# Performance work log

Measured on AMD Instinct MI355X. Metric: run time of the kernel, lower is better.

## Reference

```python
import jax, jax.numpy as jnp
import numpy as np

VOCAB = 32000
EMB = 10
HID = 256
CLS = 10
B = 1024
T = 256


def setup_inputs() -> dict:
    key = jax.random.key(0)
    ks = jax.random.split(key, 12)
    def w(k, shape):
        fan_in = shape[1]  # torch kaiming_normal_ (fan_in = size(1), gain=1 for 'linear')
        return jax.random.normal(k, shape, dtype=jnp.float32) / jnp.sqrt(jnp.float32(fan_in))
    inp = {
        "x": jax.random.randint(ks[0], (B, 1, T), 0, VOCAB, dtype=jnp.int32),
        "emb": jax.random.normal(ks[1], (VOCAB, EMB), dtype=jnp.float32),
        "Wgx": w(ks[2], (EMB, HID)), "Wgh": w(ks[3], (HID, HID)), "bg": jnp.zeros((HID,), jnp.float32),
        "Wix": w(ks[4], (EMB, HID)), "Wih": w(ks[5], (HID, HID)), "bi": jnp.zeros((HID,), jnp.float32),
        "Wfx": w(ks[6], (EMB, HID)), "Wfh": w(ks[7], (HID, HID)), "bf": jnp.zeros((HID,), jnp.float32),
        "Wox": w(ks[8], (EMB, HID)), "Woh": w(ks[9], (HID, HID)), "bo": jnp.zeros((HID,), jnp.float32),
        "Wph": w(ks[10], (HID, CLS)), "bp": jnp.zeros((CLS,), jnp.float32),
    }
    return inp


def reference(x, emb, Wgx, Wgh, bg, Wix, Wih, bi, Wfx, Wfh, bf, Wox, Woh, bo, Wph, bp):
    # Fuse the 4 gate projections into single matmuls (same math, concatenated).
    Wx = jnp.concatenate([Wgx, Wix, Wfx, Wox], axis=1)  # [EMB, 4H]
    Wh = jnp.concatenate([Wgh, Wih, Wfh, Woh], axis=1)  # [HID, 4H]
    b = jnp.concatenate([bg, bi, bf, bo], axis=0)       # [4H]
    H = Wgh.shape[0]
    tokens = x[:, 0, :].T  # [T, B] int

    def step(carry, tok_t):
        h, c = carry
        x_t = emb[tok_t]                       # [B, EMB]
        z = x_t @ Wx + h @ Wh + b              # [B, 4H]
        g = jnp.tanh(z[:, 0 * H:1 * H])
        i = jax.nn.sigmoid(z[:, 1 * H:2 * H])
        f = jax.nn.sigmoid(z[:, 2 * H:3 * H])
        o = jax.nn.sigmoid(z[:, 3 * H:4 * H])
        c = g * i + c * f
        h = jnp.tanh(c) * o
        return (h, c), None

    Bn = x.shape[0]
    h0 = jnp.zeros((Bn, H), dtype=emb.dtype)
    c0 = jnp.zeros((Bn, H), dtype=emb.dtype)
    (h, c), _ = jax.lax.scan(step, (h0, c0), tokens)
    return h @ Wph + bp  # [B, num_classes]
```

## Files before the change

### kernel.cpp

```cpp
#include <hip/hip_runtime.h>
#include <stdint.h>

#define T_STEPS 256
#define EMBD 10
#define NKIT 9
#define NBLK_K1 (64 * NKIT)
#define NBLK 256

typedef __attribute__((ext_vector_type(8))) short bf16x8;
typedef __attribute__((ext_vector_type(4))) float f32x4;
typedef __attribute__((ext_vector_type(4))) int   i32x4;

__device__ __forceinline__ unsigned short f2bf(float f) {
    union { float f; unsigned int u; } v; v.f = f;
    unsigned int u = v.u;
    unsigned int r = (u + 0x7FFFu + ((u >> 16) & 1u)) >> 16;
    return (unsigned short)r;
}
__device__ __forceinline__ float sig_fast(float x) {
    return __builtin_amdgcn_rcpf(1.0f + __builtin_amdgcn_exp2f(-1.4426950408889634f * x));
}
__device__ __forceinline__ float tanh_fast(float x) {
    return 1.0f - 2.0f * __builtin_amdgcn_rcpf(__builtin_amdgcn_exp2f(2.8853900817779268f * x) + 1.0f);
}
__device__ __forceinline__ f32x4 mfma_v(i32x4 a, i32x4 b, f32x4 c) {
    return __builtin_amdgcn_mfma_f32_16x16x32_bf16(
        __builtin_bit_cast(bf16x8, a), __builtin_bit_cast(bf16x8, b), c, 0, 0, 0);
}

__global__ __launch_bounds__(64) void build_wswz(
    const float* __restrict__ Wgx, const float* __restrict__ Wgh, const float* __restrict__ bg,
    const float* __restrict__ Wix, const float* __restrict__ Wih, const float* __restrict__ bi,
    const float* __restrict__ Wfx, const float* __restrict__ Wfh, const float* __restrict__ bf_,
    const float* __restrict__ Wox, const float* __restrict__ Woh, const float* __restrict__ bo,
    unsigned short* __restrict__ wswz, unsigned int* __restrict__ hxcz)
{
    {
        int4 z4 = {0, 0, 0, 0};
        size_t gid = (size_t)blockIdx.x * 64 + threadIdx.x;
        for (size_t i = gid; i < 131072; i += (size_t)NBLK_K1 * 64)
            ((int4*)hxcz)[i] = z4;
    }

    int g   = blockIdx.x / NKIT;
    int kit = blockIdx.x % NKIT;
    int lane = threadIdx.x;
    int n = g * 16 + (lane & 15);
    int q = n >> 8;
    int col = n & 255;
    const float* Wh = (q == 0) ? Wgh : (q == 1) ? Wih : (q == 2) ? Wfh : Woh;
    const float* Wx = (q == 0) ? Wgx : (q == 1) ? Wix : (q == 2) ? Wfx : Wox;
    const float* bb = (q == 0) ? bg  : (q == 1) ? bi  : (q == 2) ? bf_ : bo;
    int k0 = kit * 32 + (lane >> 4) * 8;

    int4 out;
    unsigned short* p = (unsigned short*)&out;
#pragma unroll
    for (int jx = 0; jx < 8; jx++) {
        int k = k0 + jx;
        float v = 0.0f;
        if (k < 256)             v = Wh[k * 256 + col];
        else if (k < 256 + EMBD) v = Wx[(k - 256) * 256 + col];
        else if (k == 266)       v = bb[col];
        p[jx] = f2bf(v);
    }
    ((int4*)wswz)[(kit * 64 + g) * 64 + lane] = out;
}

__global__ __launch_bounds__(512, 4)
void lstm_main(
    const int*   __restrict__ xtok,
    const float* __restrict__ emb,
    const float* __restrict__ Wph,
    const float* __restrict__ bp,
    const unsigned short* __restrict__ wswz,
    unsigned long long* __restrict__ hxc,
    float* __restrict__ out)
{
    __shared__ __align__(16) unsigned short A8_lds[2][64 * 8];
    __shared__ __align__(16) i32x4 B_lds[2 * 16 * 64];
    __shared__ __align__(16) unsigned int Ah_lds[16 * 132];
    __shared__ float z_lds[4 * 16 * 66];
    __shared__ float outacc[160];

    const int tid  = threadIdx.x;
    const int w    = tid >> 6;
    const int lane = tid & 63;
    const int blk  = blockIdx.x;
    const int gb   = blk & 63;
    const int hg   = blk >> 6;

    const int gate = w & 3;
    const int ntl0 = (w >> 2) * 2;

    const int m_x = tid >> 4;
    const int e_x = tid & 15;

    const int r_gm = tid >> 5;
    const int hc0  = (tid * 2) & 63;

    const i32x4* Bg = (const i32x4*)wswz;

    i32x4 breg[7][2];
    {
        const int ks[7] = {0, 1, 2, 3, 4, 7, 8};
#pragma unroll
        for (int i = 0; i < 7; i++)
#pragma unroll
            for (int jj = 0; jj < 2; jj++) {
                int ntile = gate * 16 + hg * 4 + ntl0 + jj;
                breg[i][jj] = Bg[(ks[i] * 64 + ntile) * 64 + lane];
            }
    }
    for (int i = tid; i < 2 * 16 * 64; i += 512) {
        int k   = i >> 10;
        int ntl = (i >> 6) & 15;
        int ln  = i & 63;
        int gt = ntl >> 2, j = ntl & 3;
        B_lds[i] = Bg[((5 + k) * 64 + gt * 16 + hg * 4 + j) * 64 + ln];
    }

    {
        int4 z4 = {0, 0, 0, 0};
        if (tid < 128) ((int4*)A8_lds)[tid] = z4;
    }
    __syncthreads();
    if (tid < 16) {
        A8_lds[0][(16 + tid) * 8 + 2] = 0x3F80;
        A8_lds[1][(16 + tid) * 8 + 2] = 0x3F80;
    }
    if (tid < 256 && e_x < EMBD) {
        int tok = xtok[(gb * 16 + m_x) * T_STEPS + 0];
        float v = emb[tok * EMBD + e_x];
        A8_lds[0][(m_x + 16 * (e_x >> 3)) * 8 + (e_x & 7)] = f2bf(v);
    }
    __syncthreads();

    float c0 = 0.0f, c1 = 0.0f;

    const int ah_rd = (lane & 15) * 33 + (lane >> 4);
    const int s_row  = tid >> 5;
    const int s_pair = tid & 31;
    const int rq0 = (hg + 1) & 3, rq1 = (hg + 2) & 3, rq2 = (hg + 3) & 3;

    for (int t = 0; t < T_STEPS; t++) {
        const int p = t & 1, q = (t + 1) & 1;

        float xval = 0.0f;
        const bool do_x = (t < T_STEPS - 1) && (tid < 256) && (e_x < EMBD);
        if ((t < T_STEPS - 1) && (tid < 256)) {
            int tok = xtok[(gb * 16 + m_x) * T_STEPS + (t + 1)];
            if (e_x < EMBD) xval = emb[tok * EMBD + e_x];
        }

        if (t > 0) {
            const unsigned long long* hb = hxc + (size_t)(p * 64 + gb) * 2048;
            const unsigned long long* a0 = hb + s_row * 128 + rq0 * 32 + s_pair;
            const unsigned long long* a1 = hb + s_row * 128 + rq1 * 32 + s_pair;
            const unsigned long long* a2 = hb + s_row * 128 + rq2 * 32 + s_pair;
            unsigned long long v0, v1, v2;
            asm volatile("global_load_dwordx2 %0, %3, off sc1\n\t"
                         "global_load_dwordx2 %1, %4, off sc1\n\t"
                         "global_load_dwordx2 %2, %5, off sc1\n\t"
                         "s_waitcnt vmcnt(0)"
                         : "=&v"(v0), "=&v"(v1), "=&v"(v2)
                         : "v"(a0), "v"(a1), "v"(a2) : "memory");
            int spins = 0;
            while ((unsigned int)(v0 >> 32) != (unsigned int)t && spins < 200000) {
                __builtin_amdgcn_s_sleep(1); ++spins;
                asm volatile("global_load_dwordx2 %0, %1, off sc1\n\ts_waitcnt vmcnt(0)"
                             : "=v"(v0) : "v"(a0) : "memory");
            }
            while ((unsigned int)(v1 >> 32) != (unsigned int)t && spins < 200000) {
                __builtin_amdgcn_s_sleep(1); ++spins;
                asm volatile("global_load_dwordx2 %0, %1, off sc1\n\ts_waitcnt vmcnt(0)"
                             : "=v"(v1) : "v"(a1) : "memory");
            }
            while ((unsigned int)(v2 >> 32) != (unsigned int)t && spins < 200000) {
                __builtin_amdgcn_s_sleep(1); ++spins;
                asm volatile("global_load_dwordx2 %0, %1, off sc1\n\ts_waitcnt vmcnt(0)"
                             : "=v"(v2) : "v"(a2) : "memory");
            }
            Ah_lds[s_row * 132 + rq0 * 32 + s_pair] = (unsigned int)v0;
            Ah_lds[s_row * 132 + rq1 * 32 + s_pair] = (unsigned int)v1;
            Ah_lds[s_row * 132 + rq2 * 32 + s_pair] = (unsigned int)v2;
        }
        __syncthreads();

        i32x4 af[8];
        if (t > 0) {
#pragma unroll
            for (int s = 0; s < 8; s++)
                af[s] = ((const i32x4*)Ah_lds)[ah_rd + s * 4];
        } else {
#pragma unroll
            for (int s = 0; s < 8; s++) af[s] = (i32x4){0, 0, 0, 0};
        }

        f32x4 acc0 = (f32x4){0.f, 0.f, 0.f, 0.f};
        f32x4 acc1 = (f32x4){0.f, 0.f, 0.f, 0.f};
        {
            i32x4 a8 = ((const i32x4*)A8_lds[p])[lane];
            acc0 = mfma_v(a8, breg[6][0], acc0);
            acc1 = mfma_v(a8, breg[6][1], acc1);
        }
        {
            const int ks6[6] = {0, 1, 2, 3, 4, 7};
#pragma unroll
            for (int i = 0; i < 6; i++) {
                acc0 = mfma_v(af[ks6[i]], breg[i][0], acc0);
                acc1 = mfma_v(af[ks6[i]], breg[i][1], acc1);
            }
        }
#pragma unroll
        for (int k = 0; k < 2; k++) {
            acc0 = mfma_v(af[5 + k], B_lds[(k * 16 + gate * 4 + ntl0 + 0) * 64 + lane], acc0);
            acc1 = mfma_v(af[5 + k], B_lds[(k * 16 + gate * 4 + ntl0 + 1) * 64 + lane], acc1);
        }

        {
            const int col = lane & 15, qd = lane >> 4;
#pragma unroll
            for (int rr = 0; rr < 4; rr++) {
                z_lds[(gate * 16 + qd * 4 + rr) * 66 + (ntl0 + 0) * 16 + col] = acc0[rr];
                z_lds[(gate * 16 + qd * 4 + rr) * 66 + (ntl0 + 1) * 16 + col] = acc1[rr];
            }
        }
        __syncthreads();

        float zg[4], zh[4];
#pragma unroll
        for (int g = 0; g < 4; g++) {
            const float2 zz = *(const float2*)&z_lds[(g * 16 + r_gm) * 66 + hc0];
            zg[g] = zz.x; zh[g] = zz.y;
        }
        float hh0, hh1;
        {
            float gg = tanh_fast(zg[0]), ii = sig_fast(zg[1]);
            float ff = sig_fast(zg[2]),  oo = sig_fast(zg[3]);
            float cn = gg * ii + c0 * ff; c0 = cn;
            hh0 = tanh_fast(cn) * oo;
        }
        {
            float gg = tanh_fast(zh[0]), ii = sig_fast(zh[1]);
            float ff = sig_fast(zh[2]),  oo = sig_fast(zh[3]);
            float cn = gg * ii + c1 * ff; c1 = cn;
            hh1 = tanh_fast(cn) * oo;
        }

        if (t < T_STEPS - 1) {
            unsigned int hp;
            asm("v_cvt_pk_bf16_f32 %0, %1, %2" : "=v"(hp) : "v"(hh0), "v"(hh1));
            Ah_lds[r_gm * 132 + hg * 32 + (hc0 >> 1)] = hp;
            if (do_x)
                A8_lds[q][(m_x + 16 * (e_x >> 3)) * 8 + (e_x & 7)] = f2bf(xval);
            unsigned long long pv =
                ((unsigned long long)(unsigned int)(t + 1) << 32) | (unsigned long long)hp;
            unsigned long long* dst =
                hxc + (size_t)(q * 64 + gb) * 2048 + r_gm * 128 + hg * 32 + (hc0 >> 1);
            asm volatile("global_store_dwordx2 %0, %1, off sc1"
                         :: "v"(dst), "v"(pv) : "memory");
        } else {
            if (tid < 160) outacc[tid] = 0.0f;
            __syncthreads();
            const int hcg = hg * 64 + hc0;
            float part[10];
#pragma unroll
            for (int cl = 0; cl < 10; cl++)
                part[cl] = hh0 * Wph[hcg * 10 + cl] + hh1 * Wph[(hcg + 1) * 10 + cl];
#pragma unroll
            for (int cl = 0; cl < 10; cl++)
                atomicAdd(&outacc[r_gm * 10 + cl], part[cl]);
            __syncthreads();
            if (tid < 160) {
                int m = tid / 10, cl = tid - m * 10;
                float v = outacc[tid];
                if (hg == 0) v += bp[cl];
                atomicAdd(&out[(gb * 16 + m) * 10 + cl], v);
            }
        }
    }
}

extern "C" void kernel_launch(void* const* d_in, const int* in_sizes, int n_in,
                              void* d_out, int out_size, void* d_ws, size_t ws_size,
                              hipStream_t stream) {
    const int*   x    = (const int*)  d_in[0];
    const float* emb  = (const float*)d_in[1];
    const float* Wgx  = (const float*)d_in[2];
    const float* Wgh  = (const float*)d_in[3];
    const float* bg   = (const float*)d_in[4];
    const float* Wix  = (const float*)d_in[5];
    const float* Wih  = (const float*)d_in[6];
    const float* bi   = (const float*)d_in[7];
    const float* Wfx  = (const float*)d_in[8];
    const float* Wfh  = (const float*)d_in[9];
    const float* bf_  = (const float*)d_in[10];
    const float* Wox  = (const float*)d_in[11];
    const float* Woh  = (const float*)d_in[12];
    const float* bo   = (const float*)d_in[13];
    const float* Wph  = (const float*)d_in[14];
    const float* bp   = (const float*)d_in[15];

    char* ws = (char*)d_ws;
    unsigned short*     wswz = (unsigned short*)ws;
    unsigned long long* hxc  = (unsigned long long*)(ws + 589824 + 4096);

    build_wswz<<<NBLK_K1, 64, 0, stream>>>(Wgx, Wgh, bg, Wix, Wih, bi,
                                           Wfx, Wfh, bf_, Wox, Woh, bo,
                                           wswz, (unsigned int*)hxc);
    lstm_main<<<NBLK, 512, 0, stream>>>(x, emb, Wph, bp, wswz, hxc,
                                        (float*)d_out);
}
```

Before: 585.3 us.

## Overlap cross-block h polling with MFMAs on locally produced hidden slice

```diff
diff --git a/kernel.cpp b/kernel.cpp
--- a/kernel.cpp
+++ b/kernel.cpp
@@ -66,6 +66,14 @@
     }
     ((int4*)wswz)[(kit * 64 + g) * 64 + lane] = out;
 }
+
+#define KIDX(s) ((s) == 7 ? 5 : (s))
+#define BSRC(s, j) ((s) == 5 ? B_lds[(0 * 16 + gate * 4 + ntl0 + (j)) * 64 + lane] \
+                  : (s) == 6 ? B_lds[(1 * 16 + gate * 4 + ntl0 + (j)) * 64 + lane] \
+                  : breg[KIDX(s)][(j)])
+#define DO_KIT(s) do { i32x4 a_ = ((const i32x4*)Ah_lds)[ah_rd + (s) * 4]; \
+        acc0 = mfma_v(a_, BSRC(s, 0), acc0); \
+        acc1 = mfma_v(a_, BSRC(s, 1), acc1); } while (0)
 
 __global__ __launch_bounds__(512, 4)
 void lstm_main(
@@ -153,49 +161,22 @@
             if (e_x < EMBD) xval = emb[tok * EMBD + e_x];
         }
 
+        const unsigned long long* hb = hxc + (size_t)(p * 64 + gb) * 2048;
+        const unsigned long long* a0 = hb + s_row * 128 + rq0 * 32 + s_pair;
+        const unsigned long long* a1 = hb + s_row * 128 + rq1 * 32 + s_pair;
+        const unsigned long long* a2 = hb + s_row * 128 + rq2 * 32 + s_pair;
+        unsigned long long v0 = 0, v1 = 0, v2 = 0;
+
         if (t > 0) {
-            const unsigned long long* hb = hxc + (size_t)(p * 64 + gb) * 2048;
-            const unsigned long long* a0 = hb + s_row * 128 + rq0 * 32 + s_pair;
-            const unsigned long long* a1 = hb + s_row * 128 + rq1 * 32 + s_pair;
-            const unsigned long long* a2 = hb + s_row * 128 + rq2 * 32 + s_pair;
-            unsigned long long v0, v1, v2;
             asm volatile("global_load_dwordx2 %0, %3, off sc1\n\t"
                          "global_load_dwordx2 %1, %4, off sc1\n\t"
-                         "global_load_dwordx2 %2, %5, off sc1\n\t"
-                         "s_waitcnt vmcnt(0)"
+                         "global_load_dwordx2 %2, %5, off sc1"
                          : "=&v"(v0), "=&v"(v1), "=&v"(v2)
                          : "v"(a0), "v"(a1), "v"(a2) : "memory");
-            int spins = 0;
-            while ((unsigned int)(v0 >> 32) != (unsigned int)t && spins < 200000) {
-                __builtin_amdgcn_s_sleep(1); ++spins;
-                asm volatile("global_load_dwordx2 %0, %1, off sc1\n\ts_waitcnt vmcnt(0)"
-                             : "=v"(v0) : "v"(a0) : "memory");
-            }
-            while ((unsigned int)(v1 >> 32) != (unsigned int)t && spins < 200000) {
-                __builtin_amdgcn_s_sleep(1); ++spins;
-                asm volatile("global_load_dwordx2 %0, %1, off sc1\n\ts_waitcnt vmcnt(0)"
-                             : "=v"(v1) : "v"(a1) : "memory");
-            }
-            while ((unsigned int)(v2 >> 32) != (unsigned int)t && spins < 200000) {
-                __builtin_amdgcn_s_sleep(1); ++spins;
-                asm volatile("global_load_dwordx2 %0, %1, off sc1\n\ts_waitcnt vmcnt(0)"
-                             : "=v"(v2) : "v"(a2) : "memory");
-            }
-            Ah_lds[s_row * 132 + rq0 * 32 + s_pair] = (unsigned int)v0;
-            Ah_lds[s_row * 132 + rq1 * 32 + s_pair] = (unsigned int)v1;
-            Ah_lds[s_row * 132 + rq2 * 32 + s_pair] = (unsigned int)v2;
-        }
-        __syncthreads();
-
-        i32x4 af[8];
-        if (t > 0) {
-#pragma unroll
-            for (int s = 0; s < 8; s++)
-                af[s] = ((const i32x4*)Ah_lds)[ah_rd + s * 4];
-        } else {
-#pragma unroll
-            for (int s = 0; s < 8; s++) af[s] = (i32x4){0, 0, 0, 0};
-        }
+        }
+
+        asm volatile("s_waitcnt lgkmcnt(0)" ::: "memory");
+        __builtin_amdgcn_s_barrier();
 
         f32x4 acc0 = (f32x4){0.f, 0.f, 0.f, 0.f};
         f32x4 acc1 = (f32x4){0.f, 0.f, 0.f, 0.f};
@@ -204,18 +185,39 @@
             acc0 = mfma_v(a8, breg[6][0], acc0);
             acc1 = mfma_v(a8, breg[6][1], acc1);
         }
-        {
-            const int ks6[6] = {0, 1, 2, 3, 4, 7};
-#pragma unroll
-            for (int i = 0; i < 6; i++) {
-                acc0 = mfma_v(af[ks6[i]], breg[i][0], acc0);
-                acc1 = mfma_v(af[ks6[i]], breg[i][1], acc1);
+
+        if (t > 0) {
+            if      (hg == 0) { DO_KIT(0); DO_KIT(1); }
+            else if (hg == 1) { DO_KIT(2); DO_KIT(3); }
+            else if (hg == 2) { DO_KIT(4); DO_KIT(5); }
+            else              { DO_KIT(6); DO_KIT(7); }
+
+            asm volatile("s_waitcnt vmcnt(0)"
+                         : "+v"(v0), "+v"(v1), "+v"(v2) :: "memory");
+            int spins = 0;
+            while (((unsigned)(v0 >> 32) != (unsigned)t ||
+                    (unsigned)(v1 >> 32) != (unsigned)t ||
+                    (unsigned)(v2 >> 32) != (unsigned)t) && spins < 200000) {
+                ++spins;
+                __builtin_amdgcn_s_sleep(1);
+                asm volatile("global_load_dwordx2 %0, %3, off sc1\n\t"
+                             "global_load_dwordx2 %1, %4, off sc1\n\t"
+                             "global_load_dwordx2 %2, %5, off sc1\n\t"
+                             "s_waitcnt vmcnt(0)"
+                             : "=&v"(v0), "=&v"(v1), "=&v"(v2)
+                             : "v"(a0), "v"(a1), "v"(a2) : "memory");
             }
-        }
-#pragma unroll
-        for (int k = 0; k < 2; k++) {
-            acc0 = mfma_v(af[5 + k], B_lds[(k * 16 + gate * 4 + ntl0 + 0) * 64 + lane], acc0);
-            acc1 = mfma_v(af[5 + k], B_lds[(k * 16 + gate * 4 + ntl0 + 1) * 64 + lane], acc1);
+            Ah_lds[s_row * 132 + rq0 * 32 + s_pair] = (unsigned int)v0;
+            Ah_lds[s_row * 132 + rq1 * 32 + s_pair] = (unsigned int)v1;
+            Ah_lds[s_row * 132 + rq2 * 32 + s_pair] = (unsigned int)v2;
+
+            asm volatile("s_waitcnt lgkmcnt(0)" ::: "memory");
+            __builtin_amdgcn_s_barrier();
+
+            if (hg != 0) { DO_KIT(0); DO_KIT(1); }
+            if (hg != 1) { DO_KIT(2); DO_KIT(3); }
+            if (hg != 2) { DO_KIT(4); DO_KIT(5); }
+            if (hg != 3) { DO_KIT(6); DO_KIT(7); }
         }
 
         {
```

Measured after the change: 532.2 us. 1.1x faster.
